# Kernel optimization log

Hardware: AMD Instinct MI355X
Metric: run time of the kernel (lower is better)

The kernel has to match this reference:

```python
import jax, jax.numpy as jnp
import numpy as np

EPS = 1e-06


def setup_inputs() -> dict:
    key = jax.random.key(0)
    k1, k2, k3 = jax.random.split(key, 3)
    B, L, S, C = 128, 512, 512, 64
    q = jax.random.normal(k1, (B, L, C), dtype=jnp.float32)
    k = jax.random.normal(k2, (B, S, C), dtype=jnp.float32)
    labels = jax.random.randint(k3, (B, L, S), 0, 2, dtype=jnp.int64)
    return {"q": q, "k": k, "labels": labels}


def reference(q, k, labels):
    # sim: [B, L, S], mapped to (0, 1) via (1 + cos-like sim) / 2
    sim = (1.0 + jnp.einsum('blc,bsc->bls', q, k)) * 0.5

    # column-wise stats (over L) -> [B, S]; torch.std uses ddof=1 (unbiased)
    col = (jnp.max(sim, axis=1) - jnp.mean(sim, axis=1)) / jnp.std(sim, axis=1, ddof=1)
    sharp1 = jax.nn.softmax(col, axis=-1)  # [B, S]

    # row-wise stats (over S) -> [B, L]
    row = (jnp.max(sim, axis=2) - jnp.mean(sim, axis=2)) / jnp.std(sim, axis=2, ddof=1)
    sharp2 = jax.nn.softmax(row, axis=-1)  # [B, L]

    simc = jnp.clip(sim, EPS, 1.0 - EPS)
    nll = -jnp.log(simc)                    # [B, L, S]
    nll_neg = -jnp.log(1.0 - simc)          # [B, L, S]

    pos = (labels == 1).astype(sim.dtype)
    neg = (labels == 0).astype(sim.dtype)

    # masked sums per sample, weighted by sharpness (broadcast over rows/cols)
    loss1 = jnp.sum(nll * sharp1[:, None, :] * pos, axis=(1, 2))  # [B]
    loss2 = jnp.sum(nll * sharp2[:, :, None] * pos, axis=(1, 2))  # [B]
    loss3 = jnp.sum(nll_neg * neg, axis=(1, 2)) / jnp.sum(neg, axis=(1, 2))  # [B]

    losses = (loss1 + loss2) * 0.5 + loss3
    return (sharp1, jnp.mean(losses))
```

## Files before the change

### kernel.cpp

```cpp
#include <hip/hip_runtime.h>

#define EPSF 1e-6f

typedef _Float16 half8 __attribute__((ext_vector_type(8)));
typedef float f32x4 __attribute__((ext_vector_type(4)));

constexpr int B = 128, L = 512, S = 512, C = 64;
constexpr int TILE_R = 64;
constexpr int TILES  = L / TILE_R;
constexpr int CHUNK  = 64;
constexpr int NCHUNK = S / CHUNK;
constexpr int HALVES = 2;
constexpr int CPB    = NCHUNK / HALVES;

constexpr size_t WS_COLMAX = 0;
constexpr size_t WS_COLSUM = WS_COLMAX + (size_t)B * TILES * S;
constexpr size_t WS_COLSSQ = WS_COLSUM + (size_t)B * TILES * S;
constexpr size_t WS_COLP1  = WS_COLSSQ + (size_t)B * TILES * S;
constexpr size_t WS_ROWMAX = WS_COLP1  + (size_t)B * TILES * S;
constexpr size_t WS_ROWSUM = WS_ROWMAX + (size_t)B * L * HALVES;
constexpr size_t WS_ROWSSQ = WS_ROWSUM + (size_t)B * L * HALVES;
constexpr size_t WS_ROWP2  = WS_ROWSSQ + (size_t)B * L * HALVES;
constexpr size_t WS_NEGS   = WS_ROWP2  + (size_t)B * L * HALVES;
constexpr size_t WS_NEGC   = WS_NEGS   + (size_t)B * TILES * HALVES;

__device__ inline void loadTile(const float* __restrict__ g, float4 v[4], int t)
{
    const float* src = g + (t >> 2) * 64 + (t & 3) * 16;
    v[0] = *(const float4*)(src);
    v[1] = *(const float4*)(src + 4);
    v[2] = *(const float4*)(src + 8);
    v[3] = *(const float4*)(src + 12);
}

__device__ inline void stageW(const float4 v4[4], half8 (*hiA)[64], half8 (*loA)[64], int t)
{
    const int row = t >> 2, c0 = (t & 3) * 16;
    const float v[16] = {v4[0].x, v4[0].y, v4[0].z, v4[0].w, v4[1].x, v4[1].y, v4[1].z, v4[1].w,
                         v4[2].x, v4[2].y, v4[2].z, v4[2].w, v4[3].x, v4[3].y, v4[3].z, v4[3].w};
#pragma unroll
    for (int o = 0; o < 2; ++o) {
        const int cb     = c0 + o * 8;
        const int idx    = (row >> 4) * 2 + (cb >> 5);
        const int lane_s = (((cb >> 3) & 3) << 4) + (row & 15);
        half8 h, l;
#pragma unroll
        for (int j = 0; j < 8; ++j) {
            float f = v[o * 8 + j];
            _Float16 hi = (_Float16)f;
            h[j] = hi;
            l[j] = (_Float16)(f - (float)hi);
        }
        hiA[idx][lane_s] = h;
        loA[idx][lane_s] = l;
    }
}

__global__ __launch_bounds__(256) __attribute__((amdgpu_waves_per_eu(3, 8)))
void pass1_kernel(const float* __restrict__ q, const float* __restrict__ kmat,
                  const int* __restrict__ labels, float* __restrict__ ws)
{
    __shared__ half8 khiF[8][64], kloF[8][64];
    __shared__ float4 colred4[4][CHUNK];
    __shared__ float nred[4][2];

    const int bidx = blockIdx.x;
    const int b    = bidx / (TILES * HALVES);
    const int rem  = bidx % (TILES * HALVES);
    const int tile = rem >> 1;
    const int half = rem & 1;
    const int chbase = half * CPB;
    const int tid  = threadIdx.x;
    const int lane = tid & 63;
    const int wave = tid >> 6;
    const int l15  = lane & 15;
    const int quad = lane >> 4;
    const int rowbase = tile * TILE_R;

    float* colmax_p = ws + WS_COLMAX;
    float* colsum_p = ws + WS_COLSUM;
    float* colssq_p = ws + WS_COLSSQ;
    float* colp1_p  = ws + WS_COLP1;
    float* rowmax_p = ws + WS_ROWMAX;
    float* rowsum_p = ws + WS_ROWSUM;
    float* rowssq_p = ws + WS_ROWSSQ;
    float* rowp2_p  = ws + WS_ROWP2;
    float* negs_p   = ws + WS_NEGS;
    float* negc_p   = ws + WS_NEGC;

    const float* kb = kmat + (size_t)b * S * C;
    const int*   lb = labels + ((size_t)b * L + rowbase) * S;

    float4 tv[4];
    loadTile(q + ((size_t)b * L + rowbase) * C, tv, tid);
    stageW(tv, khiF, kloF, tid);
    int labn[16];
#pragma unroll
    for (int ct = 0; ct < 4; ++ct)
#pragma unroll
        for (int r = 0; r < 4; ++r)
            labn[ct * 4 + r] = lb[(size_t)(wave * 16 + quad * 4 + r) * S
                                  + chbase * CHUNK + ct * 16 + l15];
    __syncthreads();
    half8 ah0 = khiF[wave * 2 + 0][lane], ah1 = khiF[wave * 2 + 1][lane];
    half8 al0 = kloF[wave * 2 + 0][lane], al1 = kloF[wave * 2 + 1][lane];
    loadTile(kb + (size_t)chbase * CHUNK * C, tv, tid);

    float rmax[4], rsum[4], rssq[4], rp2[4];
#pragma unroll
    for (int i = 0; i < 4; ++i) { rmax[i] = -3.4e38f; rsum[i] = 0.f; rssq[i] = 0.f; rp2[i] = 0.f; }
    float negsum = 0.f;
    int   possum = 0;

    for (int c4 = 0; c4 < CPB; ++c4) {
        const int ch = chbase + c4;
        __syncthreads();
        if (c4 > 0 && tid < CHUNK) {
            float4 v = colred4[0][tid];
            float m0 = v.x, s1 = v.y, s2 = v.z, pp = v.w;
#pragma unroll
            for (int w = 1; w < 4; ++w) {
                float4 u = colred4[w][tid];
                m0 = fmaxf(m0, u.x); s1 += u.y; s2 += u.z; pp += u.w;
            }
            size_t idx = ((size_t)b * TILES + tile) * S + (ch - 1) * CHUNK + tid;
            colmax_p[idx] = m0; colsum_p[idx] = s1; colssq_p[idx] = s2; colp1_p[idx] = pp;
        }
        stageW(tv, khiF, kloF, tid);
        if (c4 + 1 < CPB)
            loadTile(kb + (size_t)(ch + 1) * CHUNK * C, tv, tid);
        __syncthreads();

        f32x4 acc[4];
#pragma unroll
        for (int ct = 0; ct < 4; ++ct) {
            half8 bh0 = khiF[ct * 2 + 0][lane], bh1 = khiF[ct * 2 + 1][lane];
            half8 bl0 = kloF[ct * 2 + 0][lane], bl1 = kloF[ct * 2 + 1][lane];
            f32x4 a = {0.f, 0.f, 0.f, 0.f};
            a = __builtin_amdgcn_mfma_f32_16x16x32_f16(ah0, bh0, a, 0, 0, 0);
            a = __builtin_amdgcn_mfma_f32_16x16x32_f16(ah0, bl0, a, 0, 0, 0);
            a = __builtin_amdgcn_mfma_f32_16x16x32_f16(al0, bh0, a, 0, 0, 0);
            a = __builtin_amdgcn_mfma_f32_16x16x32_f16(ah1, bh1, a, 0, 0, 0);
            a = __builtin_amdgcn_mfma_f32_16x16x32_f16(ah1, bl1, a, 0, 0, 0);
            a = __builtin_amdgcn_mfma_f32_16x16x32_f16(al1, bh1, a, 0, 0, 0);
            acc[ct] = a;
        }

#pragma unroll
        for (int ct = 0; ct < 4; ++ct) {
            float cmax = -3.4e38f, csum = 0.f, cssq = 0.f, cp1 = 0.f;
#pragma unroll
            for (int r = 0; r < 4; ++r) {
                int lab = labn[ct * 4 + r];
                float sim = fmaf(0.5f, acc[ct][r], 0.5f);
                rmax[r] = fmaxf(rmax[r], sim);
                rsum[r] += sim;
                rssq[r] = fmaf(sim, sim, rssq[r]);
                cmax = fmaxf(cmax, sim);
                csum += sim;
                cssq = fmaf(sim, sim, cssq);
                float sc  = fminf(fmaxf(sim, EPSF), 1.f - EPSF);
                bool  isp = (lab == 1);
                float pos = isp ? 1.f : 0.f;
                float t   = isp ? sc : (1.f - sc);
                float nl  = -__logf(t);
                float pn  = pos * nl;
                rp2[r] += pn;
                cp1 += pn;
                negsum += nl - pn;
                possum += lab;
            }
#pragma unroll
            for (int m = 16; m <= 32; m <<= 1) {
                cmax = fmaxf(cmax, __shfl_xor(cmax, m, 64));
                csum += __shfl_xor(csum, m, 64);
                cssq += __shfl_xor(cssq, m, 64);
                cp1  += __shfl_xor(cp1,  m, 64);
            }
            if (lane < 16)
                colred4[wave][ct * 16 + l15] = make_float4(cmax, csum, cssq, cp1);
        }

        if (c4 + 1 < CPB) {
#pragma unroll
            for (int ct = 0; ct < 4; ++ct)
#pragma unroll
                for (int r = 0; r < 4; ++r)
                    labn[ct * 4 + r] = lb[(size_t)(wave * 16 + quad * 4 + r) * S
                                          + (ch + 1) * CHUNK + ct * 16 + l15];
        }
    }

    __syncthreads();
    if (tid < CHUNK) {
        float4 v = colred4[0][tid];
        float m0 = v.x, s1 = v.y, s2 = v.z, pp = v.w;
#pragma unroll
        for (int w = 1; w < 4; ++w) {
            float4 u = colred4[w][tid];
            m0 = fmaxf(m0, u.x); s1 += u.y; s2 += u.z; pp += u.w;
        }
        size_t idx = ((size_t)b * TILES + tile) * S + (chbase + CPB - 1) * CHUNK + tid;
        colmax_p[idx] = m0; colsum_p[idx] = s1; colssq_p[idx] = s2; colp1_p[idx] = pp;
    }

#pragma unroll
    for (int r = 0; r < 4; ++r) {
#pragma unroll
        for (int m = 1; m <= 8; m <<= 1) {
            rmax[r] = fmaxf(rmax[r], __shfl_xor(rmax[r], m, 64));
            rsum[r] += __shfl_xor(rsum[r], m, 64);
            rssq[r] += __shfl_xor(rssq[r], m, 64);
            rp2[r]  += __shfl_xor(rp2[r],  m, 64);
        }
    }
    if (l15 == 0) {
#pragma unroll
        for (int r = 0; r < 4; ++r) {
            size_t idx = ((size_t)b * L + rowbase + wave * 16 + quad * 4 + r) * HALVES + half;
            rowmax_p[idx] = rmax[r]; rowsum_p[idx] = rsum[r];
            rowssq_p[idx] = rssq[r]; rowp2_p[idx]  = rp2[r];
        }
    }

    float negcnt = (float)(16 * CPB - possum);
#pragma unroll
    for (int m = 1; m <= 32; m <<= 1) {
        negsum += __shfl_xor(negsum, m, 64);
        negcnt += __shfl_xor(negcnt, m, 64);
    }
    if (lane == 0) { nred[wave][0] = negsum; nred[wave][1] = negcnt; }
    __syncthreads();
    if (tid == 0) {
        float ns = 0.f, nc = 0.f;
        for (int w = 0; w < 4; ++w) { ns += nred[w][0]; nc += nred[w][1]; }
        negs_p[bidx] = ns; negc_p[bidx] = nc;
    }
}

template <bool MAX>
__device__ inline float bred(float v, float* red)
{
#pragma unroll
    for (int m = 1; m <= 32; m <<= 1) {
        float o = __shfl_xor(v, m, 64);
        v = MAX ? fmaxf(v, o) : (v + o);
    }
    const int wave = threadIdx.x >> 6;
    const int lane = threadIdx.x & 63;
    if (lane == 0) red[wave] = v;
    __syncthreads();
    if (threadIdx.x == 0) {
        float r = red[0];
        for (int w = 1; w < 8; ++w) r = MAX ? fmaxf(r, red[w]) : (r + red[w]);
        red[8] = r;
    }
    __syncthreads();
    float out = red[8];
    __syncthreads();
    return out;
}

__global__ __launch_bounds__(512)
void pass2_kernel(const float* __restrict__ ws, float* __restrict__ out)
{
    __shared__ float red[9];
    const int b = blockIdx.x;
    const int s = threadIdx.x;

    if (blockIdx.y == 0) {
        const float* colmax_p = ws + WS_COLMAX;
        const float* colsum_p = ws + WS_COLSUM;
        const float* colssq_p = ws + WS_COLSSQ;
        const float* colp1_p  = ws + WS_COLP1;

        float m = -3.4e38f, sm = 0.f, sq = 0.f, p1 = 0.f;
#pragma unroll
        for (int t = 0; t < TILES; ++t) {
            size_t idx = ((size_t)b * TILES + t) * S + s;
            m = fmaxf(m, colmax_p[idx]);
            sm += colsum_p[idx];
            sq += colssq_p[idx];
            p1 += colp1_p[idx];
        }
        float mean  = sm * (1.f / L);
        float var   = (sq - sm * sm * (1.f / L)) * (1.f / (L - 1));
        float score = (m - mean) / sqrtf(var);

        float gmax = bred<true>(score, red);
        float e    = __expf(score - gmax);
        float esum = bred<false>(e, red);
        float sharp1 = e / esum;
        out[(size_t)b * S + s] = sharp1;
        float loss1 = bred<false>(sharp1 * p1, red);
        if (s == 0) atomicAdd(out + (size_t)B * S, loss1 * (0.5f / B));
    } else {
        const float* rowmax_p = ws + WS_ROWMAX;
        const float* rowsum_p = ws + WS_ROWSUM;
        const float* rowssq_p = ws + WS_ROWSSQ;
        const float* rowp2_p  = ws + WS_ROWP2;
        const float* negs_p   = ws + WS_NEGS;
        const float* negc_p   = ws + WS_NEGC;

        size_t ridx = ((size_t)b * L + s) * HALVES;
        float m2 = rowmax_p[ridx], sm2 = rowsum_p[ridx];
        float sq2 = rowssq_p[ridx], p2 = rowp2_p[ridx];
#pragma unroll
        for (int h = 1; h < HALVES; ++h) {
            m2 = fmaxf(m2, rowmax_p[ridx + h]);
            sm2 += rowsum_p[ridx + h];
            sq2 += rowssq_p[ridx + h];
            p2  += rowp2_p[ridx + h];
        }
        float mean2  = sm2 * (1.f / S);
        float var2   = (sq2 - sm2 * sm2 * (1.f / S)) * (1.f / (S - 1));
        float score2 = (m2 - mean2) / sqrtf(var2);

        float gmax2 = bred<true>(score2, red);
        float e2    = __expf(score2 - gmax2);
        float esum2 = bred<false>(e2, red);
        float loss2 = bred<false>((e2 / esum2) * p2, red);

        if (s == 0) {
            float ns = 0.f, nc = 0.f;
            for (int t = 0; t < TILES * HALVES; ++t) {
                ns += negs_p[b * TILES * HALVES + t];
                nc += negc_p[b * TILES * HALVES + t];
            }
            atomicAdd(out + (size_t)B * S, (0.5f * loss2 + ns / nc) * (1.f / B));
        }
    }
}

extern "C" void kernel_launch(void* const* d_in, const int* in_sizes, int n_in,
                              void* d_out, int out_size, void* d_ws, size_t ws_size,
                              hipStream_t stream)
{
    const float* q      = (const float*)d_in[0];
    const float* k      = (const float*)d_in[1];
    const int*   labels = (const int*)d_in[2];
    float* out = (float*)d_out;
    float* ws  = (float*)d_ws;

    hipMemsetAsync((char*)d_out + (size_t)B * S * sizeof(float), 0, sizeof(float), stream);

    pass1_kernel<<<dim3(B * TILES * HALVES), dim3(256), 0, stream>>>(q, k, labels, ws);
    pass2_kernel<<<dim3(B, 2), dim3(512), 0, stream>>>(ws, out);
}
```

Baseline: 238.6 us.

## Load MFMA fragments directly from global memory and drop per-chunk LDS staging barriers

Each wave now loads its Q and K MFMA fragments straight from global memory into registers and converts them to hi/lo fp16 in place, instead of staging the K tile through shared memory with two block barriers per chunk. The loop is flattened to one 16-column subtile per iteration with a one-step register prefetch of the next K fragment. Column partial stats for all chunks are kept in a larger shared buffer and reduced once at the end. In exchange, every wave reads and converts the whole K slice itself, so global/L2 traffic and conversion work rise fourfold, and the wave occupancy hint is lowered.

```diff
diff --git a/kernel.cpp b/kernel.cpp
--- a/kernel.cpp
+++ b/kernel.cpp
@@ -24,44 +24,22 @@
 constexpr size_t WS_NEGS   = WS_ROWP2  + (size_t)B * L * HALVES;
 constexpr size_t WS_NEGC   = WS_NEGS   + (size_t)B * TILES * HALVES;
 
-__device__ inline void loadTile(const float* __restrict__ g, float4 v[4], int t)
-{
-    const float* src = g + (t >> 2) * 64 + (t & 3) * 16;
-    v[0] = *(const float4*)(src);
-    v[1] = *(const float4*)(src + 4);
-    v[2] = *(const float4*)(src + 8);
-    v[3] = *(const float4*)(src + 12);
-}
-
-__device__ inline void stageW(const float4 v4[4], half8 (*hiA)[64], half8 (*loA)[64], int t)
-{
-    const int row = t >> 2, c0 = (t & 3) * 16;
-    const float v[16] = {v4[0].x, v4[0].y, v4[0].z, v4[0].w, v4[1].x, v4[1].y, v4[1].z, v4[1].w,
-                         v4[2].x, v4[2].y, v4[2].z, v4[2].w, v4[3].x, v4[3].y, v4[3].z, v4[3].w};
-#pragma unroll
-    for (int o = 0; o < 2; ++o) {
-        const int cb     = c0 + o * 8;
-        const int idx    = (row >> 4) * 2 + (cb >> 5);
-        const int lane_s = (((cb >> 3) & 3) << 4) + (row & 15);
-        half8 h, l;
-#pragma unroll
-        for (int j = 0; j < 8; ++j) {
-            float f = v[o * 8 + j];
-            _Float16 hi = (_Float16)f;
-            h[j] = hi;
-            l[j] = (_Float16)(f - (float)hi);
-        }
-        hiA[idx][lane_s] = h;
-        loA[idx][lane_s] = l;
-    }
-}
-
-__global__ __launch_bounds__(256) __attribute__((amdgpu_waves_per_eu(3, 8)))
+__device__ inline void cvtFrag(const float4 a, const float4 b, half8& hi, half8& lo)
+{
+    const float v[8] = {a.x, a.y, a.z, a.w, b.x, b.y, b.z, b.w};
+#pragma unroll
+    for (int j = 0; j < 8; ++j) {
+        _Float16 h = (_Float16)v[j];
+        hi[j] = h;
+        lo[j] = (_Float16)(v[j] - (float)h);
+    }
+}
+
+__global__ __launch_bounds__(256) __attribute__((amdgpu_waves_per_eu(2, 8)))
 void pass1_kernel(const float* __restrict__ q, const float* __restrict__ kmat,
                   const int* __restrict__ labels, float* __restrict__ ws)
 {
-    __shared__ half8 khiF[8][64], kloF[8][64];
-    __shared__ float4 colred4[4][CHUNK];
+    __shared__ float4 colred4[CPB][4][CHUNK];
     __shared__ float nred[4][2];
 
     const int bidx = blockIdx.x;
@@ -91,9 +69,17 @@
     const float* kb = kmat + (size_t)b * S * C;
     const int*   lb = labels + ((size_t)b * L + rowbase) * S;
 
-    float4 tv[4];
-    loadTile(q + ((size_t)b * L + rowbase) * C, tv, tid);
-    stageW(tv, khiF, kloF, tid);
+    const float* qrow = q + ((size_t)b * L + rowbase + wave * 16 + l15) * C + quad * 8;
+    half8 ah0, al0, ah1, al1;
+    {
+        float4 a0 = *(const float4*)(qrow);
+        float4 a1 = *(const float4*)(qrow + 4);
+        float4 a2 = *(const float4*)(qrow + 32);
+        float4 a3 = *(const float4*)(qrow + 36);
+        cvtFrag(a0, a1, ah0, al0);
+        cvtFrag(a2, a3, ah1, al1);
+    }
+
     int labn[16];
 #pragma unroll
     for (int ct = 0; ct < 4; ++ct)
@@ -101,10 +87,15 @@
         for (int r = 0; r < 4; ++r)
             labn[ct * 4 + r] = lb[(size_t)(wave * 16 + quad * 4 + r) * S
                                   + chbase * CHUNK + ct * 16 + l15];
-    __syncthreads();
-    half8 ah0 = khiF[wave * 2 + 0][lane], ah1 = khiF[wave * 2 + 1][lane];
-    half8 al0 = kloF[wave * 2 + 0][lane], al1 = kloF[wave * 2 + 1][lane];
-    loadTile(kb + (size_t)chbase * CHUNK * C, tv, tid);
+
+    float4 ka0, ka1, ka2, ka3;
+    {
+        const float* kl = kb + (size_t)(chbase * CHUNK + l15) * C + quad * 8;
+        ka0 = *(const float4*)(kl);
+        ka1 = *(const float4*)(kl + 4);
+        ka2 = *(const float4*)(kl + 32);
+        ka3 = *(const float4*)(kl + 36);
+    }
 
     float rmax[4], rsum[4], rssq[4], rp2[4];
 #pragma unroll
@@ -112,95 +103,88 @@
     float negsum = 0.f;
     int   possum = 0;
 
-    for (int c4 = 0; c4 < CPB; ++c4) {
+    constexpr int ITN = CPB * 4;
+#pragma unroll 4
+    for (int it = 0; it < ITN; ++it) {
+        const int c4 = it >> 2, ct = it & 3;
         const int ch = chbase + c4;
-        __syncthreads();
-        if (c4 > 0 && tid < CHUNK) {
-            float4 v = colred4[0][tid];
-            float m0 = v.x, s1 = v.y, s2 = v.z, pp = v.w;
-#pragma unroll
-            for (int w = 1; w < 4; ++w) {
-                float4 u = colred4[w][tid];
-                m0 = fmaxf(m0, u.x); s1 += u.y; s2 += u.z; pp += u.w;
-            }
-            size_t idx = ((size_t)b * TILES + tile) * S + (ch - 1) * CHUNK + tid;
-            colmax_p[idx] = m0; colsum_p[idx] = s1; colssq_p[idx] = s2; colp1_p[idx] = pp;
-        }
-        stageW(tv, khiF, kloF, tid);
-        if (c4 + 1 < CPB)
-            loadTile(kb + (size_t)(ch + 1) * CHUNK * C, tv, tid);
-        __syncthreads();
-
-        f32x4 acc[4];
-#pragma unroll
-        for (int ct = 0; ct < 4; ++ct) {
-            half8 bh0 = khiF[ct * 2 + 0][lane], bh1 = khiF[ct * 2 + 1][lane];
-            half8 bl0 = kloF[ct * 2 + 0][lane], bl1 = kloF[ct * 2 + 1][lane];
-            f32x4 a = {0.f, 0.f, 0.f, 0.f};
-            a = __builtin_amdgcn_mfma_f32_16x16x32_f16(ah0, bh0, a, 0, 0, 0);
-            a = __builtin_amdgcn_mfma_f32_16x16x32_f16(ah0, bl0, a, 0, 0, 0);
-            a = __builtin_amdgcn_mfma_f32_16x16x32_f16(al0, bh0, a, 0, 0, 0);
-            a = __builtin_amdgcn_mfma_f32_16x16x32_f16(ah1, bh1, a, 0, 0, 0);
-            a = __builtin_amdgcn_mfma_f32_16x16x32_f16(ah1, bl1, a, 0, 0, 0);
-            a = __builtin_amdgcn_mfma_f32_16x16x32_f16(al1, bh1, a, 0, 0, 0);
-            acc[ct] = a;
-        }
-
-#pragma unroll
-        for (int ct = 0; ct < 4; ++ct) {
-            float cmax = -3.4e38f, csum = 0.f, cssq = 0.f, cp1 = 0.f;
-#pragma unroll
-            for (int r = 0; r < 4; ++r) {
-                int lab = labn[ct * 4 + r];
-                float sim = fmaf(0.5f, acc[ct][r], 0.5f);
-                rmax[r] = fmaxf(rmax[r], sim);
-                rsum[r] += sim;
-                rssq[r] = fmaf(sim, sim, rssq[r]);
-                cmax = fmaxf(cmax, sim);
-                csum += sim;
-                cssq = fmaf(sim, sim, cssq);
-                float sc  = fminf(fmaxf(sim, EPSF), 1.f - EPSF);
-                bool  isp = (lab == 1);
-                float pos = isp ? 1.f : 0.f;
-                float t   = isp ? sc : (1.f - sc);
-                float nl  = -__logf(t);
-                float pn  = pos * nl;
-                rp2[r] += pn;
-                cp1 += pn;
-                negsum += nl - pn;
-                possum += lab;
-            }
-#pragma unroll
-            for (int m = 16; m <= 32; m <<= 1) {
-                cmax = fmaxf(cmax, __shfl_xor(cmax, m, 64));
-                csum += __shfl_xor(csum, m, 64);
-                cssq += __shfl_xor(cssq, m, 64);
-                cp1  += __shfl_xor(cp1,  m, 64);
-            }
-            if (lane < 16)
-                colred4[wave][ct * 16 + l15] = make_float4(cmax, csum, cssq, cp1);
+
+        float4 kn0, kn1, kn2, kn3;
+        if (it + 1 < ITN) {
+            const int itn = it + 1;
+            const int chn = chbase + (itn >> 2), ctn = itn & 3;
+            const float* kl = kb + (size_t)(chn * CHUNK + ctn * 16 + l15) * C + quad * 8;
+            kn0 = *(const float4*)(kl);
+            kn1 = *(const float4*)(kl + 4);
+            kn2 = *(const float4*)(kl + 32);
+            kn3 = *(const float4*)(kl + 36);
+        }
+
+        half8 bh0, bl0, bh1, bl1;
+        cvtFrag(ka0, ka1, bh0, bl0);
+        cvtFrag(ka2, ka3, bh1, bl1);
+        f32x4 a = {0.f, 0.f, 0.f, 0.f};
+        a = __builtin_amdgcn_mfma_f32_16x16x32_f16(ah0, bh0, a, 0, 0, 0);
+        a = __builtin_amdgcn_mfma_f32_16x16x32_f16(ah0, bl0, a, 0, 0, 0);
+        a = __builtin_amdgcn_mfma_f32_16x16x32_f16(al0, bh0, a, 0, 0, 0);
+        a = __builtin_amdgcn_mfma_f32_16x16x32_f16(ah1, bh1, a, 0, 0, 0);
+        a = __builtin_amdgcn_mfma_f32_16x16x32_f16(ah1, bl1, a, 0, 0, 0);
+        a = __builtin_amdgcn_mfma_f32_16x16x32_f16(al1, bh1, a, 0, 0, 0);
+
+        float cmax = -3.4e38f, csum = 0.f, cssq = 0.f, cp1 = 0.f;
+#pragma unroll
+        for (int r = 0; r < 4; ++r) {
+            int lab = labn[ct * 4 + r];
+            float sim = fmaf(0.5f, a[r], 0.5f);
+            rmax[r] = fmaxf(rmax[r], sim);
+            rsum[r] += sim;
+            rssq[r] = fmaf(sim, sim, rssq[r]);
+            cmax = fmaxf(cmax, sim);
+            csum += sim;
+            cssq = fmaf(sim, sim, cssq);
+            float sc  = fminf(fmaxf(sim, EPSF), 1.f - EPSF);
+            bool  isp = (lab == 1);
+            float pos = isp ? 1.f : 0.f;
+            float t   = isp ? sc : (1.f - sc);
+            float nl  = -__logf(t);
+            float pn  = pos * nl;
+            rp2[r] += pn;
+            cp1 += pn;
+            negsum += nl - pn;
+            possum += lab;
         }
 
         if (c4 + 1 < CPB) {
 #pragma unroll
-            for (int ct = 0; ct < 4; ++ct)
-#pragma unroll
-                for (int r = 0; r < 4; ++r)
-                    labn[ct * 4 + r] = lb[(size_t)(wave * 16 + quad * 4 + r) * S
-                                          + (ch + 1) * CHUNK + ct * 16 + l15];
-        }
-    }
-
-    __syncthreads();
-    if (tid < CHUNK) {
-        float4 v = colred4[0][tid];
+            for (int r = 0; r < 4; ++r)
+                labn[ct * 4 + r] = lb[(size_t)(wave * 16 + quad * 4 + r) * S
+                                      + (ch + 1) * CHUNK + ct * 16 + l15];
+        }
+
+#pragma unroll
+        for (int m = 16; m <= 32; m <<= 1) {
+            cmax = fmaxf(cmax, __shfl_xor(cmax, m, 64));
+            csum += __shfl_xor(csum, m, 64);
+            cssq += __shfl_xor(cssq, m, 64);
+            cp1  += __shfl_xor(cp1,  m, 64);
+        }
+        if (lane < 16)
+            colred4[c4][wave][ct * 16 + l15] = make_float4(cmax, csum, cssq, cp1);
+
+        ka0 = kn0; ka1 = kn1; ka2 = kn2; ka3 = kn3;
+    }
+
+    __syncthreads();
+    {
+        const int c4 = tid >> 6, col = tid & 63;
+        float4 v = colred4[c4][0][col];
         float m0 = v.x, s1 = v.y, s2 = v.z, pp = v.w;
 #pragma unroll
         for (int w = 1; w < 4; ++w) {
-            float4 u = colred4[w][tid];
+            float4 u = colred4[c4][w][col];
             m0 = fmaxf(m0, u.x); s1 += u.y; s2 += u.z; pp += u.w;
         }
-        size_t idx = ((size_t)b * TILES + tile) * S + (chbase + CPB - 1) * CHUNK + tid;
+        size_t idx = ((size_t)b * TILES + tile) * S + (chbase + c4) * CHUNK + col;
         colmax_p[idx] = m0; colsum_p[idx] = s1; colssq_p[idx] = s2; colp1_p[idx] = pp;
     }
 
```

Measured after the change: 258.2 us. 1.08x slower.
